# Kernel tuning notes

Measured on AMD Instinct MI355X. Metric: run time of the kernel, lower is better.

## Reference

```python
import jax, jax.numpy as jnp
import numpy as np

B, C, Hh, Ww = 32, 512, 6, 40
NC = 97   # num classes; padding_idx = NC-1, start_idx = NC-2
L = 26    # label length (max_len+1); decoder tokens T = L+1 = 27


def _lstm2(x, layers):
    """2-layer unidirectional LSTM, batch_first, PyTorch gate order (i,f,g,o).
    x: (B,T,D); layers: list of (Wih, Whh, bih, bhh). Returns (B,T,H)."""
    h = x
    for (Wih, Whh, bih, bhh) in layers:
        Hd = Whh.shape[1]
        b = bih + bhh
        def step(carry, xt, Wih=Wih, Whh=Whh, b=b):
            hh, cc = carry
            g = xt @ Wih.T + hh @ Whh.T + b
            i, f, gg, o = jnp.split(g, 4, axis=-1)
            cc = jax.nn.sigmoid(f) * cc + jax.nn.sigmoid(i) * jnp.tanh(gg)
            hh = jax.nn.sigmoid(o) * jnp.tanh(cc)
            return (hh, cc), hh
        init = (jnp.zeros((h.shape[0], Hd), h.dtype), jnp.zeros((h.shape[0], Hd), h.dtype))
        _, ys = jax.lax.scan(step, init, jnp.swapaxes(h, 0, 1))
        h = jnp.swapaxes(ys, 0, 1)
    return h


def setup_inputs() -> dict:
    key = jax.random.key(0)
    it = iter(jax.random.split(key, 48))
    def nrm(shape, s=0.02):
        return jax.random.normal(next(it), shape, jnp.float32) * s
    d = {}
    d['feat'] = jax.random.normal(next(it), (B, C, Hh, Ww), jnp.float32)
    d['label'] = jax.random.randint(next(it), (B, L), 0, NC)
    d['valid_ratios'] = jax.random.uniform(next(it), (B,), jnp.float32, 0.5, 1.0)
    # encoder LSTM (2 layers, 512->512)
    for p in ['e0', 'e1']:
        d[p + '_Wih'] = nrm((4 * C, C)); d[p + '_Whh'] = nrm((4 * C, C))
        d[p + '_bih'] = jnp.zeros((4 * C,), jnp.float32); d[p + '_bhh'] = jnp.zeros((4 * C,), jnp.float32)
    d['enc_W'] = nrm((C, C)); d['enc_b'] = jnp.zeros((C,), jnp.float32)
    # attention: query 1x1 (Linear), key conv3x3, score 1x1 (Linear d->1)
    d['q_W'] = nrm((C, C)); d['q_b'] = jnp.zeros((C,), jnp.float32)
    d['k_W'] = nrm((C, C, 3, 3)); d['k_b'] = jnp.zeros((C,), jnp.float32)
    d['s_W'] = nrm((1, C)); d['s_b'] = jnp.zeros((1,), jnp.float32)
    emb = nrm((NC, C), 1.0)
    d['emb'] = emb.at[NC - 1].set(0.0)  # padding_idx row is zero
    # decoder LSTM (2 layers, 512->512)
    for p in ['d0', 'd1']:
        d[p + '_Wih'] = nrm((4 * C, C)); d[p + '_Whh'] = nrm((4 * C, C))
        d[p + '_bih'] = jnp.zeros((4 * C,), jnp.float32); d[p + '_bhh'] = jnp.zeros((4 * C,), jnp.float32)
    d['pred_W'] = nrm((NC, 3 * C)); d['pred_b'] = jnp.zeros((NC,), jnp.float32)
    return d


def reference(feat, label, valid_ratios,
              e0_Wih, e0_Whh, e0_bih, e0_bhh, e1_Wih, e1_Whh, e1_bih, e1_bhh,
              enc_W, enc_b, q_W, q_b, k_W, k_b, s_W, s_b, emb,
              d0_Wih, d0_Whh, d0_bih, d0_bhh, d1_Wih, d1_Whh, d1_bih, d1_bhh,
              pred_W, pred_b):
    # --- SAREncoder: max-pool over height, 2-layer LSTM, linear on last step ---
    feat_v = jnp.max(feat, axis=2).transpose(0, 2, 1)  # (B, W, C)
    hf = _lstm2(feat_v, [(e0_Wih, e0_Whh, e0_bih, e0_bhh), (e1_Wih, e1_Whh, e1_bih, e1_bhh)])
    holistic = hf[:, -1, :] @ enc_W.T + enc_b  # (B, C)
    # --- tokens: [holistic, embed(label)] ---
    tok = jnp.concatenate([holistic[:, None, :], emb[label]], axis=1)  # (B, T=L+1, C)
    Hid = _lstm2(tok, [(d0_Wih, d0_Whh, d0_bih, d0_bhh), (d1_Wih, d1_Whh, d1_bih, d1_bhh)])
    # --- 2D additive attention ---
    q = Hid @ q_W.T + q_b  # (B, T, C)
    k = jax.lax.conv_general_dilated(feat, k_W, (1, 1), 'SAME',
                                     dimension_numbers=('NCHW', 'OIHW', 'NCHW')) + k_b[None, :, None, None]
    t = jnp.tanh(k[:, None] + q[:, :, :, None, None])  # (B, T, C, h, w) big intermediate
    score = jnp.einsum('btchw,c->bthw', t, s_W[0]) + s_b[0]  # (B, T, h, w)
    vw = jnp.minimum(Ww, jnp.ceil(Ww * valid_ratios)).astype(jnp.int32)  # (B,)
    colmask = jnp.arange(Ww)[None, :] >= vw[:, None]  # (B, w)
    score = jnp.where(colmask[:, None, None, :], -jnp.inf, score)
    T = score.shape[1]
    aw = jax.nn.softmax(score.reshape(score.shape[0], T, -1), axis=-1).reshape(score.shape[0], T, Hh, Ww)
    attn_feat = jnp.einsum('bchw,bthw->btc', feat, aw)  # (B, T, C)
    # --- prediction (pred_concat=True); dropout is identity (deterministic) ---
    hol = jnp.broadcast_to(holistic[:, None, :], Hid.shape)
    preds = jnp.concatenate([Hid, attn_feat, hol], axis=-1) @ pred_W.T + pred_b
    return preds[:, 1:, :]  # (B, L, NC)
```

## Files before the change

### kernel.cpp

```cpp
#include <hip/hip_runtime.h>

typedef unsigned short u16;
typedef __attribute__((ext_vector_type(8))) short short8;
typedef __attribute__((ext_vector_type(4))) float floatx4;
typedef _Float16 half8 __attribute__((ext_vector_type(8)));
typedef _Float16 half2v __attribute__((ext_vector_type(2)));
typedef unsigned uint4v __attribute__((ext_vector_type(4)));

#define AGENT __HIP_MEMORY_SCOPE_AGENT
#define SENT 0x7FFF7FFFu

__device__ __forceinline__ float bf2f(u16 v) { return __uint_as_float(((unsigned)v) << 16); }
__device__ __forceinline__ u16 f2bf(float f) {
    unsigned u = __float_as_uint(f);
    unsigned r = (u + 0x7FFFu + ((u >> 16) & 1u)) >> 16;
    return (u16)r;
}
__device__ __forceinline__ float sigm_(float x) {
    return __builtin_amdgcn_rcpf(1.f + __expf(-x));
}
__device__ __forceinline__ float tanh_(float x) {
    x = fminf(fmaxf(x, -15.f), 15.f);
    float e = __expf(2.f * x);
    return (e - 1.f) * __builtin_amdgcn_rcpf(e + 1.f);
}

typedef __attribute__((address_space(1))) void gvoid_t;
typedef __attribute__((address_space(3))) void lvoid_t;
__device__ __forceinline__ void gl_lds16(const void* g, void* l) {
    __builtin_amdgcn_global_load_lds((gvoid_t*)g, (lvoid_t*)l, 16, 0, 0);
}

#define HEX_WORDS (134 * 32 * 256)

__global__ void init_k(const void* __restrict__ feat_raw, int* __restrict__ flag,
                       unsigned* __restrict__ hEx) {
    int idx = blockIdx.x * 256 + threadIdx.x;
    hEx[idx] = SENT;
    if (idx == 0) {
        const u16* p = (const u16*)feat_raw;
        int insane = 0;
        #pragma unroll
        for (int i = 0; i < 32; i += 2) {
            float x = bf2f(p[i]);
            float a = fabsf(x);
            if (!(a <= 1000.f)) insane = 1;
            if (x != 0.f && a < 1e-8f) insane = 1;
        }
        *flag = insane;
    }
}

struct SrcPtrs {
    const void* e0Wih; const void* e1Wih; const void* d0Wih; const void* d1Wih;
    const void* b0; const void* b1; const void* b2; const void* b3;
    const void* b4; const void* b5; const void* b6; const void* b7;
    const void* encW; const void* qW; const void* predW; const void* emb;
    const void* encb; const void* qb; const void* kb; const void* sW;
    const void* sb; const void* predb;
};
#define OFF_W0      0
#define OFF_W1      1048576
#define OFF_W2      2097152
#define OFF_W3      3145728
#define OFF_B       4194304
#define OFF_ENCW    4210688
#define OFF_QW      4472832
#define OFF_PREDW   4734976
#define OFF_EMB     4883968
#define OFF_ENCB    4933632
#define OFF_QB      4934144
#define OFF_KB      4934656
#define OFF_SW      4935168
#define OFF_SB      4935680
#define OFF_PREDB   4935681
#define CANON_TOTAL 4935778

__global__ __launch_bounds__(256) void canon_all(SrcPtrs S, u16* __restrict__ dst,
                                                 const int* __restrict__ flag) {
    int idx = blockIdx.x * 256 + threadIdx.x;
    if (idx >= CANON_TOTAL) return;
    const void* s; int loc;
    if (idx < OFF_B) {
        int k = idx >> 20; loc = idx & 1048575;
        s = (k == 0) ? S.e0Wih : (k == 1) ? S.e1Wih : (k == 2) ? S.d0Wih : S.d1Wih;
    } else if (idx < OFF_ENCW) {
        int r = idx - OFF_B; int k = r >> 11; loc = r & 2047;
        s = (k == 0) ? S.b0 : (k == 1) ? S.b1 : (k == 2) ? S.b2 : (k == 3) ? S.b3
          : (k == 4) ? S.b4 : (k == 5) ? S.b5 : (k == 6) ? S.b6 : S.b7;
    } else if (idx < OFF_QW)    { s = S.encW;  loc = idx - OFF_ENCW; }
    else if (idx < OFF_PREDW)   { s = S.qW;    loc = idx - OFF_QW; }
    else if (idx < OFF_EMB)     { s = S.predW; loc = idx - OFF_PREDW; }
    else if (idx < OFF_ENCB)    { s = S.emb;   loc = idx - OFF_EMB; }
    else if (idx < OFF_QB)      { s = S.encb;  loc = idx - OFF_ENCB; }
    else if (idx < OFF_KB)      { s = S.qb;    loc = idx - OFF_QB; }
    else if (idx < OFF_SW)      { s = S.kb;    loc = idx - OFF_KB; }
    else if (idx < OFF_SB)      { s = S.sW;    loc = idx - OFF_SW; }
    else if (idx < OFF_PREDB)   { s = S.sb;    loc = idx - OFF_SB; }
    else                        { s = S.predb; loc = idx - OFF_PREDB; }
    dst[idx] = (*flag) ? f2bf(((const float*)s)[loc]) : ((const u16*)s)[loc];
}

__global__ __launch_bounds__(64) void canonf_k(const void* __restrict__ src, float* __restrict__ dst,
                                               int n, const int* __restrict__ flag) {
    int i = blockIdx.x * 64 + threadIdx.x;
    if (i >= n) return;
    dst[i] = (*flag) ? ((const float*)src)[i] : bf2f(((const u16*)src)[i]);
}

__device__ __forceinline__ float rdf(const void* p, long i, int fl) {
    return fl ? ((const float*)p)[i] : bf2f(((const u16*)p)[i]);
}

__global__ __launch_bounds__(256) void featv_k(const void* __restrict__ feat, u16* __restrict__ featv,
                                               const int* __restrict__ flag) {
    const int fl = *flag;
    int idx = blockIdx.x * 256 + threadIdx.x;
    int c = idx & 511;
    int r = idx >> 9;
    int w = r % 40, b = r / 40;
    float mx = -1e30f;
    long base = ((long)(b * 512 + c) * 6) * 40 + w;
    #pragma unroll
    for (int h = 0; h < 6; h++) mx = fmaxf(mx, rdf(feat, base + h * 40, fl));
    featv[idx] = f2bf(mx);
}

__global__ __launch_bounds__(256) void padfeat_k(const void* __restrict__ feat, u16* __restrict__ featP,
                                                 const int* __restrict__ flag) {
    const int fl = *flag;
    int idx = blockIdx.x * 256 + threadIdx.x;
    int c = idx & 511;
    int r = idx >> 9;
    int wp = r % 42; int r2 = r / 42;
    int hp = r2 & 7; int b = r2 >> 3;
    u16 v = 0;
    if (hp >= 1 && hp <= 6 && wp >= 1 && wp <= 40) {
        long si = ((long)(b * 512 + c) * 6 + (hp - 1)) * 40 + (wp - 1);
        v = fl ? f2bf(((const float*)feat)[si]) : ((const u16*)feat)[si];
    }
    featP[idx] = v;
}

__global__ __launch_bounds__(256) void w2_k(const void* __restrict__ kW, u16* __restrict__ W2,
                                            const int* __restrict__ flag) {
    int idx = blockIdx.x * 256 + threadIdx.x;
    int co = idx / 4608;
    int r = idx % 4608;
    int kh = r / 1536;
    int r2 = r % 1536;
    int kw = r2 / 512;
    int ci = r2 & 511;
    long si = ((long)(co * 512 + ci) * 3 + kh) * 3 + kw;
    W2[idx] = (*flag) ? f2bf(((const float*)kW)[si]) : ((const u16*)kW)[si];
}

__global__ __launch_bounds__(256) void wq3_all(
    const void* __restrict__ s0, const void* __restrict__ s1,
    const void* __restrict__ s2, const void* __restrict__ s3,
    _Float16* __restrict__ d0, _Float16* __restrict__ d1,
    _Float16* __restrict__ d2, _Float16* __restrict__ d3,
    const int* __restrict__ flag)
{
    int gb = blockIdx.x;
    int id = gb >> 9;
    const void* W = (id == 0) ? s0 : (id == 1) ? s1 : (id == 2) ? s2 : s3;
    _Float16* D = (id == 0) ? d0 : (id == 1) ? d1 : (id == 2) ? d2 : d3;
    int o = (gb & 511) * 256 + threadIdx.x;
    int t = o & 511;
    int c = (o >> 9) & 31;
    int j = o >> 14;
    int rid = t >> 1, hf = t & 1;
    int n = (rid >> 6) * 512 + j * 64 + (rid & 63);
    int k = hf * 256 + c * 8;
    int fl = *flag;
    _Float16* dst = D + (long)o * 8;
    #pragma unroll
    for (int jj = 0; jj < 8; jj++) {
        long si = (long)n * 512 + k + jj;
        float v = fl ? ((const float*)W)[si] : bf2f(((const u16*)W)[si]);
        dst[jj] = (_Float16)v;
    }
}

__global__ __launch_bounds__(256) void gemm_nt_f32(
    const u16* __restrict__ A, int lda,
    const u16* __restrict__ Bw,
    const u16* __restrict__ bias0, const u16* __restrict__ bias1,
    float* __restrict__ C, int M, int N, int K, int ldc)
{
    __shared__ __align__(16) u16 As[64][40];
    __shared__ __align__(16) u16 Bs[64][40];
    const int tid = threadIdx.x;
    const int bn = blockIdx.x, bm = blockIdx.y;
    const int l = tid & 63, wid = tid >> 6;
    const int wm = wid >> 1, wn = wid & 1;
    const int lr = tid >> 2, lc = (tid & 3) * 8;
    const int l15 = l & 15, lq = l >> 4;

    floatx4 acc00 = (floatx4)(0.f), acc01 = (floatx4)(0.f), acc10 = (floatx4)(0.f), acc11 = (floatx4)(0.f);

    int am = bm * 64 + lr; if (am > M - 1) am = M - 1;
    const u16* Ap = A + (long)am * lda + lc;
    const u16* Bp = Bw + (long)(bn * 64 + lr) * K + lc;

    for (int k0 = 0; k0 < K; k0 += 32) {
        *(short8*)&As[lr][lc] = *(const short8*)(Ap + k0);
        *(short8*)&Bs[lr][lc] = *(const short8*)(Bp + k0);
        __syncthreads();
        short8 af0 = *(const short8*)&As[wm * 32 + l15][lq * 8];
        short8 af1 = *(const short8*)&As[wm * 32 + 16 + l15][lq * 8];
        short8 bf0 = *(const short8*)&Bs[wn * 32 + l15][lq * 8];
        short8 bf1 = *(const short8*)&Bs[wn * 32 + 16 + l15][lq * 8];
        acc00 = __builtin_amdgcn_mfma_f32_16x16x32_bf16(af0, bf0, acc00, 0, 0, 0);
        acc01 = __builtin_amdgcn_mfma_f32_16x16x32_bf16(af0, bf1, acc01, 0, 0, 0);
        acc10 = __builtin_amdgcn_mfma_f32_16x16x32_bf16(af1, bf0, acc10, 0, 0, 0);
        acc11 = __builtin_amdgcn_mfma_f32_16x16x32_bf16(af1, bf1, acc11, 0, 0, 0);
        __syncthreads();
    }
    floatx4 accs[2][2] = {{acc00, acc01}, {acc10, acc11}};
    #pragma unroll
    for (int i = 0; i < 2; i++)
        #pragma unroll
        for (int j = 0; j < 2; j++)
            #pragma unroll
            for (int r = 0; r < 4; r++) {
                int gm = bm * 64 + wm * 32 + i * 16 + lq * 4 + r;
                int gn = bn * 64 + wn * 32 + j * 16 + l15;
                if (gm < M) {
                    float v = accs[i][j][r];
                    if (bias0) v += bf2f(bias0[gn]);
                    if (bias1) v += bf2f(bias1[gn]);
                    C[(long)gm * ldc + gn] = v;
                }
            }
}

__global__ __launch_bounds__(512) void conv_gemm(
    const u16* __restrict__ featP, const u16* __restrict__ W2,
    const u16* __restrict__ kb, u16* __restrict__ kmap)
{
    __shared__ __align__(16) u16 As[4][128][32];
    __shared__ __align__(16) u16 Bs[4][128][32];
    const int tid = threadIdx.x;
    int bm = blockIdx.x * 8 + (blockIdx.y & 7);
    int bn = blockIdx.y >> 3;
    if (bm >= 60) return;
    const int wv = tid >> 6, l = tid & 63;
    const int wm = wv >> 2, wn = wv & 3;
    const int l15 = l & 15, lq = l >> 4;
    const int ch = ((l & 3) ^ ((l >> 3) & 3)) * 8;

    int ar = bm * 128 + wv * 16 + (l >> 2);
    int ab = ar / 240, ahw = ar % 240;
    const u16* ga = featP + ((long)(ab * 8 + ahw / 40) * 42 + (ahw % 40)) * 512 + ch;
    const u16* gb = W2 + (long)(bn * 128 + wv * 16 + (l >> 2)) * 4608 + ch;

    floatx4 acc[4][2];
    #pragma unroll
    for (int i = 0; i < 4; i++)
        #pragma unroll
        for (int j = 0; j < 2; j++) acc[i][j] = (floatx4)(0.f);

    auto stage = [&](int k0, int pb) {
        int kh = k0 / 1536;
        int rem = k0 - kh * 1536;
        int aoff = (kh * 42 + (rem >> 9)) * 512 + (rem & 511);
        gl_lds16(ga + aoff, &As[pb][wv * 16][0]);
        gl_lds16(gb + k0, &Bs[pb][wv * 16][0]);
    };

    const int rs = (lq ^ ((l15 >> 1) & 3)) * 8;

    auto compute = [&](int cur) {
        short8 af[4], bf[2];
        #pragma unroll
        for (int i = 0; i < 4; i++) af[i] = *(const short8*)&As[cur][wm * 64 + i * 16 + l15][rs];
        #pragma unroll
        for (int j = 0; j < 2; j++) bf[j] = *(const short8*)&Bs[cur][wn * 32 + j * 16 + l15][rs];
        #pragma unroll
        for (int i = 0; i < 4; i++)
            #pragma unroll
            for (int j = 0; j < 2; j++)
                acc[i][j] = __builtin_amdgcn_mfma_f32_16x16x32_bf16(af[i], bf[j], acc[i][j], 0, 0, 0);
    };

    stage(0, 0); stage(32, 1); stage(64, 2);
    for (int k = 0; k < 142; k++) {
        asm volatile("s_waitcnt vmcnt(4)" ::: "memory");
        __builtin_amdgcn_s_barrier();
        asm volatile("" ::: "memory");
        if (k < 141) stage((k + 3) * 32, (k + 3) & 3);
        compute(k & 3);
    }
    asm volatile("s_waitcnt vmcnt(2)" ::: "memory");
    __builtin_amdgcn_s_barrier();
    asm volatile("" ::: "memory");
    compute(2);
    asm volatile("s_waitcnt vmcnt(0)" ::: "memory");
    __builtin_amdgcn_s_barrier();
    asm volatile("" ::: "memory");
    compute(3);

    #pragma unroll
    for (int i = 0; i < 4; i++)
        #pragma unroll
        for (int j = 0; j < 2; j++)
            #pragma unroll
            for (int r = 0; r < 4; r++) {
                int row = bm * 128 + wm * 64 + i * 16 + lq * 4 + r;
                int col = bn * 128 + wn * 32 + j * 16 + l15;
                kmap[(long)row * 512 + col] = f2bf(acc[i][j][r] + bf2f(kb[col]));
            }
}

#define WL(F) F(0) F(1) F(2) F(3) F(4) F(5) F(6) F(7) F(8) F(9) F(10) F(11) F(12) F(13) F(14) F(15) \
              F(16) F(17) F(18) F(19) F(20) F(21) F(22) F(23) F(24) F(25) F(26) F(27) F(28) F(29) F(30) F(31)
#define WLA(F) F(0,0) F(1,1) F(2,2) F(3,3) F(4,0) F(5,1) F(6,2) F(7,3) \
               F(8,0) F(9,1) F(10,2) F(11,3) F(12,0) F(13,1) F(14,2) F(15,3) \
               F(16,0) F(17,1) F(18,2) F(19,3) F(20,0) F(21,1) F(22,2) F(23,3) \
               F(24,0) F(25,1) F(26,2) F(27,3) F(28,0) F(29,1) F(30,2) F(31,3)
#define WDECL(i) half8 w##i = wp8[(long)(j * 32 + i) * 512 + tid];
#define WPIN(i)  asm volatile("" : "+v"(w##i));
#define DOTC(i,k) { \
    half8 hv = *(const half8*)&hS2[(hf * 2 + (i / 16)) * 136 + (i % 16) * 8]; \
    a##k = __builtin_amdgcn_fdot2(__builtin_shufflevector(hv, hv, 0, 1), __builtin_shufflevector(w##i, w##i, 0, 1), a##k, false); \
    a##k = __builtin_amdgcn_fdot2(__builtin_shufflevector(hv, hv, 2, 3), __builtin_shufflevector(w##i, w##i, 2, 3), a##k, false); \
    a##k = __builtin_amdgcn_fdot2(__builtin_shufflevector(hv, hv, 4, 5), __builtin_shufflevector(w##i, w##i, 4, 5), a##k, false); \
    a##k = __builtin_amdgcn_fdot2(__builtin_shufflevector(hv, hv, 6, 7), __builtin_shufflevector(w##i, w##i, 6, 7), a##k, false); }

__global__ __launch_bounds__(512) __attribute__((amdgpu_waves_per_eu(2, 2))) void lstm_sync(
    const float* __restrict__ xpre, const _Float16* __restrict__ Wq3,
    u16* __restrict__ seq_out, float* __restrict__ f32_out,
    unsigned* __restrict__ hExT, int T, int f32_ld)
{
    const int i_ = blockIdx.x;
    const int slot = i_ >> 3;
    const int b = (i_ & 7) * 4 + (slot & 3);
    const int j = slot >> 2;
    const int tid = threadIdx.x;
    const int hf = tid & 1;

    __shared__ __align__(16) _Float16 hS2[4 * 136];
    __shared__ float part[512];

    const half8* wp8 = (const half8*)Wq3;
    WL(WDECL)
    WL(WPIN)
    float cst = 0.f;

    for (int t = 0; t < T; t++) {
        float xi = 0.f, xf = 0.f, xg = 0.f, xo = 0.f;
        if (tid < 64) {
            const float* xp = xpre + ((long)b * T + t) * 2048 + j * 64 + tid;
            xi = xp[0]; xf = xp[512]; xg = xp[1024]; xo = xp[1536];
        }
        float a0 = 0.f, a1 = 0.f, a2 = 0.f, a3 = 0.f;
        if (t > 0) {
            if (tid < 64) {
                const unsigned* src = &hExT[((long)(t - 1) * 32 + b) * 256 + tid * 4];
                unsigned v0, v1, v2, v3;
                do {
                    v0 = __hip_atomic_load(src + 0, __ATOMIC_RELAXED, AGENT);
                    v1 = __hip_atomic_load(src + 1, __ATOMIC_RELAXED, AGENT);
                    v2 = __hip_atomic_load(src + 2, __ATOMIC_RELAXED, AGENT);
                    v3 = __hip_atomic_load(src + 3, __ATOMIC_RELAXED, AGENT);
                } while (v0 == SENT || v1 == SENT || v2 == SENT || v3 == SENT);
                uint4v v; v.x = v0; v.y = v1; v.z = v2; v.w = v3;
                *(uint4v*)&hS2[(tid >> 4) * 136 + (tid & 15) * 8] = v;
            }
            __syncthreads();
            WLA(DOTC)
        }
        part[tid] = (a0 + a1) + (a2 + a3);
        __syncthreads();
        if (tid < 64) {
            float gi = xi + part[(0   + tid) * 2] + part[(0   + tid) * 2 + 1];
            float gf = xf + part[(64  + tid) * 2] + part[(64  + tid) * 2 + 1];
            float gg = xg + part[(128 + tid) * 2] + part[(128 + tid) * 2 + 1];
            float go = xo + part[(192 + tid) * 2] + part[(192 + tid) * 2 + 1];
            cst = sigm_(gf) * cst + sigm_(gi) * tanh_(gg);
            float h = sigm_(go) * tanh_(cst);
            float hlo = __shfl(h, tid * 2);
            float hhi = __shfl(h, tid * 2 + 1);
            if (t + 1 < T && tid < 32) {
                half2v hp; hp[0] = (_Float16)hlo; hp[1] = (_Float16)hhi;
                __hip_atomic_store(&hExT[((long)t * 32 + b) * 256 + j * 32 + tid],
                                   *(unsigned*)&hp, __ATOMIC_RELAXED, AGENT);
            }
            asm volatile("" ::: "memory");
            long so = ((long)b * T + t) * 512 + j * 64 + tid;
            seq_out[so] = f2bf(h);
            if (f32_out) f32_out[((long)b * T + t) * f32_ld + j * 64 + tid] = h;
        }
    }
}

__global__ __launch_bounds__(256) void tok_k(
    const float* __restrict__ holf, const u16* __restrict__ cemb,
    const int* __restrict__ label, u16* __restrict__ tok)
{
    int idx = blockIdx.x * 256 + threadIdx.x;
    int c = idx & 511;
    int m = idx >> 9;
    int b = m / 27, t = m % 27;
    float v;
    if (t == 0) v = holf[(long)b * 512 + c];
    else v = bf2f(cemb[(long)label[b * 26 + (t - 1)] * 512 + c]);
    tok[idx] = f2bf(v);
}

__global__ __launch_bounds__(256) void score_k(
    const float* __restrict__ q, const u16* __restrict__ kmap,
    const u16* __restrict__ sW, const u16* __restrict__ sb,
    const float* __restrict__ vr, float* __restrict__ aw)
{
    int blk = blockIdx.x;
    int xcd = blk & 7, rest = blk >> 3;
    int bq = rest & 3, t = rest >> 2;
    int b = xcd * 4 + bq;
    int bt = b * 27 + t;
    int tid = threadIdx.x, wv = tid >> 6, ln = tid & 63;

    __shared__ float sc[240];
    __shared__ float red[256];

    float qr[8], sr[8];
    const float* qp = q + (long)bt * 512 + ln * 8;
    #pragma unroll
    for (int i = 0; i < 8; i++) qr[i] = qp[i];
    #pragma unroll
    for (int i = 0; i < 8; i++) sr[i] = bf2f(sW[ln * 8 + i]);

    const u16* kb_ = kmap + (long)b * 240 * 512;
    for (int r = wv * 60; r < wv * 60 + 60; r++) {
        short8 kv = *(const short8*)(kb_ + (long)r * 512 + ln * 8);
        float acc = 0.f;
        #pragma unroll
        for (int i = 0; i < 8; i++) {
            float x = bf2f((u16)kv[i]) + qr[i];
            acc = fmaf(sr[i], tanh_(x), acc);
        }
        #pragma unroll
        for (int m = 32; m > 0; m >>= 1) acc += __shfl_xor(acc, m);
        if (ln == 0) sc[r] = acc;
    }
    __syncthreads();

    float scv = -INFINITY, ex = 0.f;
    if (tid < 240) {
        float rr = vr[b];
        int vw = (int)ceilf(40.f * rr);
        if (vw > 40) vw = 40;
        int wcol = tid % 40;
        scv = (wcol >= vw) ? -INFINITY : (sc[tid] + bf2f(sb[0]));
    }
    red[tid] = scv;
    __syncthreads();
    for (int s = 128; s > 0; s >>= 1) {
        if (tid < s) red[tid] = fmaxf(red[tid], red[tid + s]);
        __syncthreads();
    }
    float mx = red[0];
    __syncthreads();
    if (tid < 240) ex = (scv == -INFINITY) ? 0.f : __expf(scv - mx);
    red[tid] = ex;
    __syncthreads();
    for (int s = 128; s > 0; s >>= 1) {
        if (tid < s) red[tid] += red[tid + s];
        __syncthreads();
    }
    float inv = __builtin_amdgcn_rcpf(red[0]);
    if (tid < 240) aw[(long)bt * 240 + tid] = ex * inv;
}

__global__ __launch_bounds__(256) void attn_k(
    const void* __restrict__ feat, const float* __restrict__ aw,
    float* __restrict__ concat, const int* __restrict__ flag)
{
    const int fl = *flag;
    int b = blockIdx.x >> 3;
    int cc = (blockIdx.x & 7) * 64;
    int tid = threadIdx.x;
    __shared__ float awS[27 * 240];
    __shared__ u16 fS[64 * 240];
    for (int i = tid; i < 27 * 240; i += 256) awS[i] = aw[(long)b * 27 * 240 + i];
    long fbase = ((long)b * 512 + cc) * 240;
    for (int i = tid; i < 64 * 240; i += 256)
        fS[i] = fl ? f2bf(((const float*)feat)[fbase + i]) : ((const u16*)feat)[fbase + i];
    __syncthreads();
    for (int item = tid; item < 64 * 27; item += 256) {
        int c = item / 27, t = item % 27;
        const u16* fp = &fS[c * 240];
        const float* ap = &awS[t * 240];
        float acc = 0.f;
        for (int hw = 0; hw < 240; hw++) acc = fmaf(bf2f(fp[hw]), ap[hw], acc);
        concat[((long)(b * 27 + t)) * 1536 + 512 + cc + c] = acc;
    }
}

__global__ __launch_bounds__(256) void pred_k(
    const float* __restrict__ concat, const float* __restrict__ holf,
    const u16* __restrict__ pW, const u16* __restrict__ pb,
    void* __restrict__ out, const int* __restrict__ flag)
{
    int m0 = blockIdx.x * 4;
    int tid = threadIdx.x;
    const int fl = *flag;
    __shared__ float aS[4][1024];
    __shared__ float hS[4][512];
    for (int i = tid; i < 4 * 1024; i += 256)
        aS[i / 1024][i % 1024] = concat[(long)(m0 + i / 1024) * 1536 + (i % 1024)];
    for (int i = tid; i < 4 * 512; i += 256) {
        int m = m0 + i / 512;
        hS[i / 512][i % 512] = holf[(long)(m / 27) * 512 + (i % 512)];
    }
    __syncthreads();
    int r = tid >> 6;
    int nb = tid & 63;
    int m = m0 + r;
    int b = m / 27, t = m % 27;
    for (int n = nb; n < 97; n += 64) {
        const u16* wp = pW + (long)n * 1536;
        float acc = 0.f;
        for (int k = 0; k < 1024; k++) acc = fmaf(aS[r][k], bf2f(wp[k]), acc);
        for (int k = 0; k < 512; k++) acc = fmaf(hS[r][k], bf2f(wp[1024 + k]), acc);
        acc += bf2f(pb[n]);
        if (t > 0) {
            long o = ((long)(b * 26 + (t - 1))) * 97 + n;
            if (fl) ((float*)out)[o] = acc;
            else    ((u16*)out)[o] = f2bf(acc);
        }
    }
}

extern "C" void kernel_launch(void* const* d_in, const int* in_sizes, int n_in,
                              void* d_out, int out_size, void* d_ws, size_t ws_size,
                              hipStream_t stream) {
    (void)in_sizes; (void)n_in; (void)out_size; (void)ws_size;
    const void* feat_r = d_in[0];
    const int*  label  = (const int*)d_in[1];
    const void* vr_r   = d_in[2];

    char* w = (char*)d_ws;
    size_t off = 0;
    auto alloc = [&](size_t bytes) -> void* {
        void* p = w + off;
        off = (off + bytes + 63) & ~(size_t)63;
        return p;
    };
    int*   flag    = (int*)  alloc(4);
    unsigned* hEx  = (unsigned*)alloc((size_t)HEX_WORDS * 4);
    u16*   canon   = (u16*)  alloc((size_t)CANON_TOTAL * 2);
    float* cvr     = (float*)alloc(32ull * 4);
    u16*   featv   = (u16*)  alloc(655360ull * 2);
    float* xpre    = (float*)alloc(2621440ull * 4);
    u16*   seq0    = (u16*)  alloc(655360ull * 2);
    u16*   seq1    = (u16*)  alloc(655360ull * 2);
    u16*   tok     = (u16*)  alloc(442368ull * 2);
    u16*   seqd0   = (u16*)  alloc(442368ull * 2);
    u16*   Hid     = (u16*)  alloc(442368ull * 2);
    float* holf    = (float*)alloc(16384ull * 4);
    float* qf      = (float*)alloc(442368ull * 4);
    u16*   featP   = (u16*)  alloc(5505024ull * 2);
    u16*   W2      = (u16*)  alloc(2359296ull * 2);
    float* aw      = (float*)alloc(207360ull * 4);
    float* concat  = (float*)alloc(1327104ull * 4);
    _Float16* Wq[4];
    for (int i = 0; i < 4; i++) Wq[i] = (_Float16*)alloc(1048576ull * 2);
    u16*   kmap    = (u16*)xpre;

    unsigned* hEx0 = hEx;
    unsigned* hEx1 = hEx + 40ull * 8192;
    unsigned* hEx2 = hEx + 80ull * 8192;
    unsigned* hEx3 = hEx + 107ull * 8192;

    u16* cW0    = canon + OFF_W0;
    u16* cW1    = canon + OFF_W1;
    u16* cW2    = canon + OFF_W2;
    u16* cW3    = canon + OFF_W3;
    u16* cb0    = canon + OFF_B;
    u16* cencW  = canon + OFF_ENCW;
    u16* cqW    = canon + OFF_QW;
    u16* cpredW = canon + OFF_PREDW;
    u16* cemb   = canon + OFF_EMB;
    u16* cencb  = canon + OFF_ENCB;
    u16* cqb    = canon + OFF_QB;
    u16* ckb    = canon + OFF_KB;
    u16* csW    = canon + OFF_SW;
    u16* csb    = canon + OFF_SB;
    u16* cpredb = canon + OFF_PREDB;

    init_k<<<dim3(HEX_WORDS / 256), 256, 0, stream>>>(feat_r, flag, hEx);
    SrcPtrs S;
    S.e0Wih = d_in[3];  S.e1Wih = d_in[7];  S.d0Wih = d_in[20]; S.d1Wih = d_in[24];
    S.b0 = d_in[5];  S.b1 = d_in[6];  S.b2 = d_in[9];  S.b3 = d_in[10];
    S.b4 = d_in[22]; S.b5 = d_in[23]; S.b6 = d_in[26]; S.b7 = d_in[27];
    S.encW = d_in[11]; S.qW = d_in[13]; S.predW = d_in[28]; S.emb = d_in[19];
    S.encb = d_in[12]; S.qb = d_in[14]; S.kb = d_in[16]; S.sW = d_in[17];
    S.sb = d_in[18]; S.predb = d_in[29];
    canon_all<<<dim3((CANON_TOTAL + 255) / 256), 256, 0, stream>>>(S, canon, flag);
    canonf_k<<<dim3(1), 64, 0, stream>>>(vr_r, cvr, 32, flag);
    w2_k<<<dim3(9216), 256, 0, stream>>>(d_in[15], W2, flag);
    wq3_all<<<dim3(2048), 256, 0, stream>>>(d_in[4], d_in[8], d_in[21], d_in[25],
                                            Wq[0], Wq[1], Wq[2], Wq[3], flag);

    featv_k  <<<dim3(2560), 256, 0, stream>>>(feat_r, featv, flag);
    padfeat_k<<<dim3(21504), 256, 0, stream>>>(feat_r, featP, flag);

    gemm_nt_f32<<<dim3(32, 20), 256, 0, stream>>>(featv, 512, cW0, cb0 + 0 * 2048, cb0 + 1 * 2048, xpre, 1280, 2048, 512, 2048);
    lstm_sync<<<dim3(256), 512, 0, stream>>>(xpre, Wq[0], seq0, nullptr, hEx0, 40, 0);
    gemm_nt_f32<<<dim3(32, 20), 256, 0, stream>>>(seq0, 512, cW1, cb0 + 2 * 2048, cb0 + 3 * 2048, xpre, 1280, 2048, 512, 2048);
    lstm_sync<<<dim3(256), 512, 0, stream>>>(xpre, Wq[1], seq1, nullptr, hEx1, 40, 0);
    gemm_nt_f32<<<dim3(8, 1), 256, 0, stream>>>(seq1 + 39 * 512, 40 * 512, cencW, cencb, nullptr, holf, 32, 512, 512, 512);

    tok_k<<<dim3(1728), 256, 0, stream>>>(holf, cemb, label, tok);
    gemm_nt_f32<<<dim3(32, 14), 256, 0, stream>>>(tok, 512, cW2, cb0 + 4 * 2048, cb0 + 5 * 2048, xpre, 864, 2048, 512, 2048);
    lstm_sync<<<dim3(256), 512, 0, stream>>>(xpre, Wq[2], seqd0, nullptr, hEx2, 27, 0);
    gemm_nt_f32<<<dim3(32, 14), 256, 0, stream>>>(seqd0, 512, cW3, cb0 + 6 * 2048, cb0 + 7 * 2048, xpre, 864, 2048, 512, 2048);
    lstm_sync<<<dim3(256), 512, 0, stream>>>(xpre, Wq[3], Hid, concat, hEx3, 27, 1536);

    gemm_nt_f32<<<dim3(8, 14), 256, 0, stream>>>(Hid, 512, cqW, cqb, nullptr, qf, 864, 512, 512, 512);
    conv_gemm<<<dim3(8, 32), 512, 0, stream>>>(featP, W2, ckb, kmap);
    score_k<<<dim3(864), 256, 0, stream>>>(qf, kmap, csW, csb, cvr, aw);
    attn_k<<<dim3(256), 256, 0, stream>>>(feat_r, aw, concat, flag);

    pred_k<<<dim3(216), 256, 0, stream>>>(concat, holf, cpredW, cpredb, d_out, flag);
}
```

Before: 815.6 us.

## Poll mirrored hidden-state buffer with vector sc0 loads in LSTM inter-block exchange

Result: slower. 907.8 us (+11.3%).

```diff
diff --git a/kernel.cpp b/kernel.cpp
--- a/kernel.cpp
+++ b/kernel.cpp
@@ -357,17 +357,27 @@
         }
         float a0 = 0.f, a1 = 0.f, a2 = 0.f, a3 = 0.f;
         if (t > 0) {
-            if (tid < 64) {
-                const unsigned* src = &hExT[((long)(t - 1) * 32 + b) * 256 + tid * 4];
-                unsigned v0, v1, v2, v3;
-                do {
-                    v0 = __hip_atomic_load(src + 0, __ATOMIC_RELAXED, AGENT);
-                    v1 = __hip_atomic_load(src + 1, __ATOMIC_RELAXED, AGENT);
-                    v2 = __hip_atomic_load(src + 2, __ATOMIC_RELAXED, AGENT);
-                    v3 = __hip_atomic_load(src + 3, __ATOMIC_RELAXED, AGENT);
-                } while (v0 == SENT || v1 == SENT || v2 == SENT || v3 == SENT);
-                uint4v v; v.x = v0; v.y = v1; v.z = v2; v.w = v3;
-                *(uint4v*)&hS2[(tid >> 4) * 136 + (tid & 15) * 8] = v;
+            if (tid >= 64 && tid < 128) {
+                const int ln = tid - 64;
+                const unsigned* srcB = &hExT[((long)(t - 1) * 32 + b) * 256 + ln * 4];
+                const unsigned* srcA = srcB + HEX_WORDS;
+                uint4v q;
+                int it = 0;
+                for (;;) {
+                    asm volatile("global_load_dwordx4 %0, %1, off sc0" : "=v"(q) : "v"(srcA));
+                    asm volatile("s_waitcnt vmcnt(0)" ::: "memory");
+                    if (q.x != SENT && q.y != SENT && q.z != SENT && q.w != SENT) break;
+                    if ((++it & 3) == 0) {
+                        unsigned v0 = __hip_atomic_load(srcB + 0, __ATOMIC_RELAXED, AGENT);
+                        unsigned v1 = __hip_atomic_load(srcB + 1, __ATOMIC_RELAXED, AGENT);
+                        unsigned v2 = __hip_atomic_load(srcB + 2, __ATOMIC_RELAXED, AGENT);
+                        unsigned v3 = __hip_atomic_load(srcB + 3, __ATOMIC_RELAXED, AGENT);
+                        if (v0 != SENT && v1 != SENT && v2 != SENT && v3 != SENT) {
+                            q.x = v0; q.y = v1; q.z = v2; q.w = v3; break;
+                        }
+                    }
+                }
+                *(uint4v*)&hS2[(ln >> 4) * 136 + (ln & 15) * 8] = q;
             }
             __syncthreads();
             WLA(DOTC)
@@ -385,8 +395,10 @@
             float hhi = __shfl(h, tid * 2 + 1);
             if (t + 1 < T && tid < 32) {
                 half2v hp; hp[0] = (_Float16)hlo; hp[1] = (_Float16)hhi;
-                __hip_atomic_store(&hExT[((long)t * 32 + b) * 256 + j * 32 + tid],
-                                   *(unsigned*)&hp, __ATOMIC_RELAXED, AGENT);
+                unsigned word = *(unsigned*)&hp;
+                long off = ((long)t * 32 + b) * 256 + j * 32 + tid;
+                ((volatile unsigned*)hExT)[HEX_WORDS + off] = word;
+                __hip_atomic_store(&hExT[off], word, __ATOMIC_RELAXED, AGENT);
             }
             asm volatile("" ::: "memory");
             long so = ((long)b * T + t) * 512 + j * 64 + tid;
@@ -550,7 +562,7 @@
         return p;
     };
     int*   flag    = (int*)  alloc(4);
-    unsigned* hEx  = (unsigned*)alloc((size_t)HEX_WORDS * 4);
+    unsigned* hEx  = (unsigned*)alloc((size_t)HEX_WORDS * 2 * 4);
     u16*   canon   = (u16*)  alloc((size_t)CANON_TOTAL * 2);
     float* cvr     = (float*)alloc(32ull * 4);
     u16*   featv   = (u16*)  alloc(655360ull * 2);
@@ -591,7 +603,7 @@
     u16* csb    = canon + OFF_SB;
     u16* cpredb = canon + OFF_PREDB;
 
-    init_k<<<dim3(HEX_WORDS / 256), 256, 0, stream>>>(feat_r, flag, hEx);
+    init_k<<<dim3(HEX_WORDS * 2 / 256), 256, 0, stream>>>(feat_r, flag, hEx);
     SrcPtrs S;
     S.e0Wih = d_in[3];  S.e1Wih = d_in[7];  S.d0Wih = d_in[20]; S.d1Wih = d_in[24];
     S.b0 = d_in[5];  S.b1 = d_in[6];  S.b2 = d_in[9];  S.b3 = d_in[10];
```

## Fuse two stacked LSTM layers into one wavefront-pipelined persistent kernel

Applied to the files above, without the earlier changes.

Measured after the change: 1.743 ms. 114% more time.

```diff
diff --git a/kernel.cpp b/kernel.cpp
--- a/kernel.cpp
+++ b/kernel.cpp
@@ -155,17 +155,19 @@
     W2[idx] = (*flag) ? f2bf(((const float*)kW)[si]) : ((const u16*)kW)[si];
 }
 
-__global__ __launch_bounds__(256) void wq3_all(
+__global__ __launch_bounds__(256) void wq6_all(
     const void* __restrict__ s0, const void* __restrict__ s1,
     const void* __restrict__ s2, const void* __restrict__ s3,
+    const void* __restrict__ s4, const void* __restrict__ s5,
     _Float16* __restrict__ d0, _Float16* __restrict__ d1,
     _Float16* __restrict__ d2, _Float16* __restrict__ d3,
+    _Float16* __restrict__ d4, _Float16* __restrict__ d5,
     const int* __restrict__ flag)
 {
     int gb = blockIdx.x;
     int id = gb >> 9;
-    const void* W = (id == 0) ? s0 : (id == 1) ? s1 : (id == 2) ? s2 : s3;
-    _Float16* D = (id == 0) ? d0 : (id == 1) ? d1 : (id == 2) ? d2 : d3;
+    const void* W = (id == 0) ? s0 : (id == 1) ? s1 : (id == 2) ? s2 : (id == 3) ? s3 : (id == 4) ? s4 : s5;
+    _Float16* D = (id == 0) ? d0 : (id == 1) ? d1 : (id == 2) ? d2 : (id == 3) ? d3 : (id == 4) ? d4 : d5;
     int o = (gb & 511) * 256 + threadIdx.x;
     int t = o & 511;
     int c = (o >> 9) & 31;
@@ -320,19 +322,35 @@
                F(8,0) F(9,1) F(10,2) F(11,3) F(12,0) F(13,1) F(14,2) F(15,3) \
                F(16,0) F(17,1) F(18,2) F(19,3) F(20,0) F(21,1) F(22,2) F(23,3) \
                F(24,0) F(25,1) F(26,2) F(27,3) F(28,0) F(29,1) F(30,2) F(31,3)
-#define WDECL(i) half8 w##i = wp8[(long)(j * 32 + i) * 512 + tid];
-#define WPIN(i)  asm volatile("" : "+v"(w##i));
-#define DOTC(i,k) { \
-    half8 hv = *(const half8*)&hS2[(hf * 2 + (i / 16)) * 136 + (i % 16) * 8]; \
-    a##k = __builtin_amdgcn_fdot2(__builtin_shufflevector(hv, hv, 0, 1), __builtin_shufflevector(w##i, w##i, 0, 1), a##k, false); \
-    a##k = __builtin_amdgcn_fdot2(__builtin_shufflevector(hv, hv, 2, 3), __builtin_shufflevector(w##i, w##i, 2, 3), a##k, false); \
-    a##k = __builtin_amdgcn_fdot2(__builtin_shufflevector(hv, hv, 4, 5), __builtin_shufflevector(w##i, w##i, 4, 5), a##k, false); \
-    a##k = __builtin_amdgcn_fdot2(__builtin_shufflevector(hv, hv, 6, 7), __builtin_shufflevector(w##i, w##i, 6, 7), a##k, false); }
-
-__global__ __launch_bounds__(512) __attribute__((amdgpu_waves_per_eu(2, 2))) void lstm_sync(
-    const float* __restrict__ xpre, const _Float16* __restrict__ Wq3,
-    u16* __restrict__ seq_out, float* __restrict__ f32_out,
-    unsigned* __restrict__ hExT, int T, int f32_ld)
+#define WDECL3(i) half8 wa##i = wpa[(long)(j * 32 + i) * 512 + tid]; \
+                  half8 wb##i = wpb[(long)(j * 32 + i) * 512 + tid]; \
+                  half8 wc##i = wpc[(long)(j * 32 + i) * 512 + tid];
+#define WPIN3(i)  asm volatile("" : "+v"(wa##i)); asm volatile("" : "+v"(wb##i)); asm volatile("" : "+v"(wc##i));
+#define DOTA(i,k) { \
+    half8 hv = *(const half8*)&hX[(hf * 2 + (i / 16)) * 136 + (i % 16) * 8]; \
+    a##k = __builtin_amdgcn_fdot2(__builtin_shufflevector(hv, hv, 0, 1), __builtin_shufflevector(wa##i, wa##i, 0, 1), a##k, false); \
+    a##k = __builtin_amdgcn_fdot2(__builtin_shufflevector(hv, hv, 2, 3), __builtin_shufflevector(wa##i, wa##i, 2, 3), a##k, false); \
+    a##k = __builtin_amdgcn_fdot2(__builtin_shufflevector(hv, hv, 4, 5), __builtin_shufflevector(wa##i, wa##i, 4, 5), a##k, false); \
+    a##k = __builtin_amdgcn_fdot2(__builtin_shufflevector(hv, hv, 6, 7), __builtin_shufflevector(wa##i, wa##i, 6, 7), a##k, false); }
+#define DOTI(i,k) { \
+    half8 hv = *(const half8*)&hX[(hf * 2 + (i / 16)) * 136 + (i % 16) * 8]; \
+    c##k = __builtin_amdgcn_fdot2(__builtin_shufflevector(hv, hv, 0, 1), __builtin_shufflevector(wc##i, wc##i, 0, 1), c##k, false); \
+    c##k = __builtin_amdgcn_fdot2(__builtin_shufflevector(hv, hv, 2, 3), __builtin_shufflevector(wc##i, wc##i, 2, 3), c##k, false); \
+    c##k = __builtin_amdgcn_fdot2(__builtin_shufflevector(hv, hv, 4, 5), __builtin_shufflevector(wc##i, wc##i, 4, 5), c##k, false); \
+    c##k = __builtin_amdgcn_fdot2(__builtin_shufflevector(hv, hv, 6, 7), __builtin_shufflevector(wc##i, wc##i, 6, 7), c##k, false); }
+#define DOTB(i,k) { \
+    half8 hv = *(const half8*)&hH[(hf * 2 + (i / 16)) * 136 + (i % 16) * 8]; \
+    c##k = __builtin_amdgcn_fdot2(__builtin_shufflevector(hv, hv, 0, 1), __builtin_shufflevector(wb##i, wb##i, 0, 1), c##k, false); \
+    c##k = __builtin_amdgcn_fdot2(__builtin_shufflevector(hv, hv, 2, 3), __builtin_shufflevector(wb##i, wb##i, 2, 3), c##k, false); \
+    c##k = __builtin_amdgcn_fdot2(__builtin_shufflevector(hv, hv, 4, 5), __builtin_shufflevector(wb##i, wb##i, 4, 5), c##k, false); \
+    c##k = __builtin_amdgcn_fdot2(__builtin_shufflevector(hv, hv, 6, 7), __builtin_shufflevector(wb##i, wb##i, 6, 7), c##k, false); }
+
+__global__ __launch_bounds__(512) __attribute__((amdgpu_waves_per_eu(2, 2))) void lstm_fused2(
+    const float* __restrict__ xpre, const _Float16* __restrict__ WhA,
+    const _Float16* __restrict__ WhB, const _Float16* __restrict__ WiB,
+    const u16* __restrict__ bB0, const u16* __restrict__ bB1,
+    u16* __restrict__ seq2, float* __restrict__ f32_out,
+    unsigned* __restrict__ hExA, unsigned* __restrict__ hExB, int T, int f32_ld)
 {
     const int i_ = blockIdx.x;
     const int slot = i_ >> 3;
@@ -341,24 +359,38 @@
     const int tid = threadIdx.x;
     const int hf = tid & 1;
 
-    __shared__ __align__(16) _Float16 hS2[4 * 136];
-    __shared__ float part[512];
-
-    const half8* wp8 = (const half8*)Wq3;
-    WL(WDECL)
-    WL(WPIN)
-    float cst = 0.f;
-
-    for (int t = 0; t < T; t++) {
+    __shared__ __align__(16) _Float16 hX[4 * 136];
+    __shared__ __align__(16) _Float16 hH[4 * 136];
+    __shared__ float partA[512];
+    __shared__ float partB[512];
+
+    const half8* wpa = (const half8*)WhA;
+    const half8* wpb = (const half8*)WhB;
+    const half8* wpc = (const half8*)WiB;
+    WL(WDECL3)
+    WL(WPIN3)
+
+    float bBi = 0.f, bBf = 0.f, bBg = 0.f, bBo = 0.f;
+    if (tid >= 64 && tid < 128) {
+        int ln = tid - 64;
+        bBi = bf2f(bB0[0 * 512 + j * 64 + ln]) + bf2f(bB1[0 * 512 + j * 64 + ln]);
+        bBf = bf2f(bB0[1 * 512 + j * 64 + ln]) + bf2f(bB1[1 * 512 + j * 64 + ln]);
+        bBg = bf2f(bB0[2 * 512 + j * 64 + ln]) + bf2f(bB1[2 * 512 + j * 64 + ln]);
+        bBo = bf2f(bB0[3 * 512 + j * 64 + ln]) + bf2f(bB1[3 * 512 + j * 64 + ln]);
+    }
+
+    float cstA = 0.f, cstB = 0.f;
+
+    for (int t = 0; t <= T; t++) {
         float xi = 0.f, xf = 0.f, xg = 0.f, xo = 0.f;
-        if (tid < 64) {
+        if (t < T && tid < 64) {
             const float* xp = xpre + ((long)b * T + t) * 2048 + j * 64 + tid;
             xi = xp[0]; xf = xp[512]; xg = xp[1024]; xo = xp[1536];
         }
-        float a0 = 0.f, a1 = 0.f, a2 = 0.f, a3 = 0.f;
         if (t > 0) {
-            if (tid < 64) {
-                const unsigned* src = &hExT[((long)(t - 1) * 32 + b) * 256 + tid * 4];
+            if (tid >= 64 && tid < 128) {
+                const int ln = tid - 64;
+                const unsigned* src = &hExA[((long)(t - 1) * 32 + b) * 256 + ln * 4];
                 unsigned v0, v1, v2, v3;
                 do {
                     v0 = __hip_atomic_load(src + 0, __ATOMIC_RELAXED, AGENT);
@@ -367,32 +399,67 @@
                     v3 = __hip_atomic_load(src + 3, __ATOMIC_RELAXED, AGENT);
                 } while (v0 == SENT || v1 == SENT || v2 == SENT || v3 == SENT);
                 uint4v v; v.x = v0; v.y = v1; v.z = v2; v.w = v3;
-                *(uint4v*)&hS2[(tid >> 4) * 136 + (tid & 15) * 8] = v;
+                *(uint4v*)&hX[(ln >> 4) * 136 + (ln & 15) * 8] = v;
+            }
+            if (t > 1 && tid >= 128 && tid < 192) {
+                const int ln = tid - 128;
+                const unsigned* src = &hExB[((long)(t - 2) * 32 + b) * 256 + ln * 4];
+                unsigned v0, v1, v2, v3;
+                do {
+                    v0 = __hip_atomic_load(src + 0, __ATOMIC_RELAXED, AGENT);
+                    v1 = __hip_atomic_load(src + 1, __ATOMIC_RELAXED, AGENT);
+                    v2 = __hip_atomic_load(src + 2, __ATOMIC_RELAXED, AGENT);
+                    v3 = __hip_atomic_load(src + 3, __ATOMIC_RELAXED, AGENT);
+                } while (v0 == SENT || v1 == SENT || v2 == SENT || v3 == SENT);
+                uint4v v; v.x = v0; v.y = v1; v.z = v2; v.w = v3;
+                *(uint4v*)&hH[(ln >> 4) * 136 + (ln & 15) * 8] = v;
             }
             __syncthreads();
-            WLA(DOTC)
         }
-        part[tid] = (a0 + a1) + (a2 + a3);
+        float a0 = 0.f, a1 = 0.f, a2 = 0.f, a3 = 0.f;
+        if (t > 0 && t < T) { WLA(DOTA) }
+        partA[tid] = (a0 + a1) + (a2 + a3);
+        float c0 = 0.f, c1 = 0.f, c2 = 0.f, c3 = 0.f;
+        if (t > 0) { WLA(DOTI) }
+        if (t > 1) { WLA(DOTB) }
+        partB[tid] = (c0 + c1) + (c2 + c3);
         __syncthreads();
-        if (tid < 64) {
-            float gi = xi + part[(0   + tid) * 2] + part[(0   + tid) * 2 + 1];
-            float gf = xf + part[(64  + tid) * 2] + part[(64  + tid) * 2 + 1];
-            float gg = xg + part[(128 + tid) * 2] + part[(128 + tid) * 2 + 1];
-            float go = xo + part[(192 + tid) * 2] + part[(192 + tid) * 2 + 1];
-            cst = sigm_(gf) * cst + sigm_(gi) * tanh_(gg);
-            float h = sigm_(go) * tanh_(cst);
+        if (t < T && tid < 64) {
+            float gi = xi + partA[(0   + tid) * 2] + partA[(0   + tid) * 2 + 1];
+            float gf = xf + partA[(64  + tid) * 2] + partA[(64  + tid) * 2 + 1];
+            float gg = xg + partA[(128 + tid) * 2] + partA[(128 + tid) * 2 + 1];
+            float go = xo + partA[(192 + tid) * 2] + partA[(192 + tid) * 2 + 1];
+            cstA = sigm_(gf) * cstA + sigm_(gi) * tanh_(gg);
+            float h = sigm_(go) * tanh_(cstA);
             float hlo = __shfl(h, tid * 2);
             float hhi = __shfl(h, tid * 2 + 1);
-            if (t + 1 < T && tid < 32) {
+            if (tid < 32) {
                 half2v hp; hp[0] = (_Float16)hlo; hp[1] = (_Float16)hhi;
-                __hip_atomic_store(&hExT[((long)t * 32 + b) * 256 + j * 32 + tid],
+                __hip_atomic_store(&hExA[((long)t * 32 + b) * 256 + j * 32 + tid],
+                                   *(unsigned*)&hp, __ATOMIC_RELAXED, AGENT);
+            }
+        }
+        if (t > 0 && tid >= 64 && tid < 128) {
+            const int ln = tid - 64;
+            float gi = bBi + partB[(0   + ln) * 2] + partB[(0   + ln) * 2 + 1];
+            float gf = bBf + partB[(64  + ln) * 2] + partB[(64  + ln) * 2 + 1];
+            float gg = bBg + partB[(128 + ln) * 2] + partB[(128 + ln) * 2 + 1];
+            float go = bBo + partB[(192 + ln) * 2] + partB[(192 + ln) * 2 + 1];
+            cstB = sigm_(gf) * cstB + sigm_(gi) * tanh_(gg);
+            float h = sigm_(go) * tanh_(cstB);
+            float hlo = __shfl(h, ln * 2);
+            float hhi = __shfl(h, ln * 2 + 1);
+            if (ln < 32 && t < T) {
+                half2v hp; hp[0] = (_Float16)hlo; hp[1] = (_Float16)hhi;
+                __hip_atomic_store(&hExB[((long)(t - 1) * 32 + b) * 256 + j * 32 + ln],
                                    *(unsigned*)&hp, __ATOMIC_RELAXED, AGENT);
             }
             asm volatile("" ::: "memory");
-            long so = ((long)b * T + t) * 512 + j * 64 + tid;
-            seq_out[so] = f2bf(h);
-            if (f32_out) f32_out[((long)b * T + t) * f32_ld + j * 64 + tid] = h;
+            long so = ((long)b * T + (t - 1)) * 512 + j * 64 + ln;
+            seq2[so] = f2bf(h);
+            if (f32_out) f32_out[((long)b * T + (t - 1)) * f32_ld + j * 64 + ln] = h;
         }
+        __syncthreads();
     }
 }
 
@@ -555,10 +622,8 @@
     float* cvr     = (float*)alloc(32ull * 4);
     u16*   featv   = (u16*)  alloc(655360ull * 2);
     float* xpre    = (float*)alloc(2621440ull * 4);
-    u16*   seq0    = (u16*)  alloc(655360ull * 2);
     u16*   seq1    = (u16*)  alloc(655360ull * 2);
     u16*   tok     = (u16*)  alloc(442368ull * 2);
-    u16*   seqd0   = (u16*)  alloc(442368ull * 2);
     u16*   Hid     = (u16*)  alloc(442368ull * 2);
     float* holf    = (float*)alloc(16384ull * 4);
     float* qf      = (float*)alloc(442368ull * 4);
@@ -566,8 +631,8 @@
     u16*   W2      = (u16*)  alloc(2359296ull * 2);
     float* aw      = (float*)alloc(207360ull * 4);
     float* concat  = (float*)alloc(1327104ull * 4);
-    _Float16* Wq[4];
-    for (int i = 0; i < 4; i++) Wq[i] = (_Float16*)alloc(1048576ull * 2);
+    _Float16* Wq[6];
+    for (int i = 0; i < 6; i++) Wq[i] = (_Float16*)alloc(1048576ull * 2);
     u16*   kmap    = (u16*)xpre;
 
     unsigned* hEx0 = hEx;
@@ -576,9 +641,7 @@
     unsigned* hEx3 = hEx + 107ull * 8192;
 
     u16* cW0    = canon + OFF_W0;
-    u16* cW1    = canon + OFF_W1;
     u16* cW2    = canon + OFF_W2;
-    u16* cW3    = canon + OFF_W3;
     u16* cb0    = canon + OFF_B;
     u16* cencW  = canon + OFF_ENCW;
     u16* cqW    = canon + OFF_QW;
@@ -602,23 +665,23 @@
     canon_all<<<dim3((CANON_TOTAL + 255) / 256), 256, 0, stream>>>(S, canon, flag);
     canonf_k<<<dim3(1), 64, 0, stream>>>(vr_r, cvr, 32, flag);
     w2_k<<<dim3(9216), 256, 0, stream>>>(d_in[15], W2, flag);
-    wq3_all<<<dim3(2048), 256, 0, stream>>>(d_in[4], d_in[8], d_in[21], d_in[25],
-                                            Wq[0], Wq[1], Wq[2], Wq[3], flag);
+    wq6_all<<<dim3(3072), 256, 0, stream>>>(d_in[4], d_in[8], d_in[21], d_in[25], d_in[7], d_in[24],
+                                            Wq[0], Wq[1], Wq[2], Wq[3], Wq[4], Wq[5], flag);
 
     featv_k  <<<dim3(2560), 256, 0, stream>>>(feat_r, featv, flag);
     padfeat_k<<<dim3(21504), 256, 0, stream>>>(feat_r, featP, flag);
 
     gemm_nt_f32<<<dim3(32, 20), 256, 0, stream>>>(featv, 512, cW0, cb0 + 0 * 2048, cb0 + 1 * 2048, xpre, 1280, 2048, 512, 2048);
-    lstm_sync<<<dim3(256), 512, 0, stream>>>(xpre, Wq[0], seq0, nullptr, hEx0, 40, 0);
-    gemm_nt_f32<<<dim3(32, 20), 256, 0, stream>>>(seq0, 512, cW1, cb0 + 2 * 2048, cb0 + 3 * 2048, xpre, 1280, 2048, 512, 2048);
-    lstm_sync<<<dim3(256), 512, 0, stream>>>(xpre, Wq[1], seq1, nullptr, hEx1, 40, 0);
+    lstm_fused2<<<dim3(256), 512, 0, stream>>>(xpre, Wq[0], Wq[1], Wq[4],
+                                               cb0 + 2 * 2048, cb0 + 3 * 2048,
+                                               seq1, nullptr, hEx0, hEx1, 40, 0);
     gemm_nt_f32<<<dim3(8, 1), 256, 0, stream>>>(seq1 + 39 * 512, 40 * 512, cencW, cencb, nullptr, holf, 32, 512, 512, 512);
 
     tok_k<<<dim3(1728), 256, 0, stream>>>(holf, cemb, label, tok);
     gemm_nt_f32<<<dim3(32, 14), 256, 0, stream>>>(tok, 512, cW2, cb0 + 4 * 2048, cb0 + 5 * 2048, xpre, 864, 2048, 512, 2048);
-    lstm_sync<<<dim3(256), 512, 0, stream>>>(xpre, Wq[2], seqd0, nullptr, hEx2, 27, 0);
-    gemm_nt_f32<<<dim3(32, 14), 256, 0, stream>>>(seqd0, 512, cW3, cb0 + 6 * 2048, cb0 + 7 * 2048, xpre, 864, 2048, 512, 2048);
-    lstm_sync<<<dim3(256), 512, 0, stream>>>(xpre, Wq[3], Hid, concat, hEx3, 27, 1536);
+    lstm_fused2<<<dim3(256), 512, 0, stream>>>(xpre, Wq[2], Wq[3], Wq[5],
+                                               cb0 + 6 * 2048, cb0 + 7 * 2048,
+                                               Hid, concat, hEx2, hEx3, 27, 1536);
 
     gemm_nt_f32<<<dim3(8, 14), 256, 0, stream>>>(Hid, 512, cqW, cqb, nullptr, qf, 864, 512, 512, 512);
     conv_gemm<<<dim3(8, 32), 512, 0, stream>>>(featP, W2, ckb, kmap);
```

## Co-schedule key conv GEMM with first encoder LSTM in one launch

Applied to the files above, without the earlier changes.

Measured after the change: 859.0 us. 1.05x slower.

```diff
diff --git a/kernel.cpp b/kernel.cpp
--- a/kernel.cpp
+++ b/kernel.cpp
@@ -236,15 +236,15 @@
             }
 }
 
-__global__ __launch_bounds__(512) void conv_gemm(
+__device__ __forceinline__ void conv_body(
     const u16* __restrict__ featP, const u16* __restrict__ W2,
-    const u16* __restrict__ kb, u16* __restrict__ kmap)
+    const u16* __restrict__ kb, u16* __restrict__ kmap, int bx, int by)
 {
     __shared__ __align__(16) u16 As[4][128][32];
     __shared__ __align__(16) u16 Bs[4][128][32];
     const int tid = threadIdx.x;
-    int bm = blockIdx.x * 8 + (blockIdx.y & 7);
-    int bn = blockIdx.y >> 3;
+    int bm = bx * 8 + (by & 7);
+    int bn = by >> 3;
     if (bm >= 60) return;
     const int wv = tid >> 6, l = tid & 63;
     const int wm = wv >> 2, wn = wv & 3;
@@ -329,7 +329,7 @@
     a##k = __builtin_amdgcn_fdot2(__builtin_shufflevector(hv, hv, 4, 5), __builtin_shufflevector(w##i, w##i, 4, 5), a##k, false); \
     a##k = __builtin_amdgcn_fdot2(__builtin_shufflevector(hv, hv, 6, 7), __builtin_shufflevector(w##i, w##i, 6, 7), a##k, false); }
 
-__global__ __launch_bounds__(512) __attribute__((amdgpu_waves_per_eu(2, 2))) void lstm_sync(
+__device__ __forceinline__ void lstm_body(
     const float* __restrict__ xpre, const _Float16* __restrict__ Wq3,
     u16* __restrict__ seq_out, float* __restrict__ f32_out,
     unsigned* __restrict__ hExT, int T, int f32_ld)
@@ -396,6 +396,28 @@
     }
 }
 
+__global__ __launch_bounds__(512) __attribute__((amdgpu_waves_per_eu(2, 2))) void lstm_sync(
+    const float* __restrict__ xpre, const _Float16* __restrict__ Wq3,
+    u16* __restrict__ seq_out, float* __restrict__ f32_out,
+    unsigned* __restrict__ hExT, int T, int f32_ld)
+{
+    lstm_body(xpre, Wq3, seq_out, f32_out, hExT, T, f32_ld);
+}
+
+__global__ __launch_bounds__(512, 4) void enc1_conv(
+    const float* __restrict__ xpre, const _Float16* __restrict__ Wq3,
+    u16* __restrict__ seq_out, unsigned* __restrict__ hExT,
+    const u16* __restrict__ featP, const u16* __restrict__ W2,
+    const u16* __restrict__ kb, u16* __restrict__ kmap)
+{
+    if (blockIdx.x < 256) {
+        lstm_body(xpre, Wq3, seq_out, nullptr, hExT, 40, 0);
+    } else {
+        int c = blockIdx.x - 256;
+        conv_body(featP, W2, kb, kmap, c & 7, c >> 3);
+    }
+}
+
 __global__ __launch_bounds__(256) void tok_k(
     const float* __restrict__ holf, const u16* __restrict__ cemb,
     const int* __restrict__ label, u16* __restrict__ tok)
@@ -566,9 +588,9 @@
     u16*   W2      = (u16*)  alloc(2359296ull * 2);
     float* aw      = (float*)alloc(207360ull * 4);
     float* concat  = (float*)alloc(1327104ull * 4);
+    u16*   kmap    = (u16*)  alloc(3932160ull * 2);
     _Float16* Wq[4];
     for (int i = 0; i < 4; i++) Wq[i] = (_Float16*)alloc(1048576ull * 2);
-    u16*   kmap    = (u16*)xpre;
 
     unsigned* hEx0 = hEx;
     unsigned* hEx1 = hEx + 40ull * 8192;
@@ -609,7 +631,7 @@
     padfeat_k<<<dim3(21504), 256, 0, stream>>>(feat_r, featP, flag);
 
     gemm_nt_f32<<<dim3(32, 20), 256, 0, stream>>>(featv, 512, cW0, cb0 + 0 * 2048, cb0 + 1 * 2048, xpre, 1280, 2048, 512, 2048);
-    lstm_sync<<<dim3(256), 512, 0, stream>>>(xpre, Wq[0], seq0, nullptr, hEx0, 40, 0);
+    enc1_conv<<<dim3(512), 512, 0, stream>>>(xpre, Wq[0], seq0, hEx0, featP, W2, ckb, kmap);
     gemm_nt_f32<<<dim3(32, 20), 256, 0, stream>>>(seq0, 512, cW1, cb0 + 2 * 2048, cb0 + 3 * 2048, xpre, 1280, 2048, 512, 2048);
     lstm_sync<<<dim3(256), 512, 0, stream>>>(xpre, Wq[1], seq1, nullptr, hEx1, 40, 0);
     gemm_nt_f32<<<dim3(8, 1), 256, 0, stream>>>(seq1 + 39 * 512, 40 * 512, cencW, cencb, nullptr, holf, 32, 512, 512, 512);
@@ -621,7 +643,6 @@
     lstm_sync<<<dim3(256), 512, 0, stream>>>(xpre, Wq[3], Hid, concat, hEx3, 27, 1536);
 
     gemm_nt_f32<<<dim3(8, 14), 256, 0, stream>>>(Hid, 512, cqW, cqb, nullptr, qf, 864, 512, 512, 512);
-    conv_gemm<<<dim3(8, 32), 512, 0, stream>>>(featP, W2, ckb, kmap);
     score_k<<<dim3(864), 256, 0, stream>>>(qf, kmap, csW, csb, cvr, aw);
     attn_k<<<dim3(256), 256, 0, stream>>>(feat_r, aw, concat, flag);
 
```
